# Optimization experiments

Measured on AMD Instinct MI355X. Metric: run time of the kernel, lower is better.

## Reference

```python
import jax, jax.numpy as jnp
import numpy as np

D_MODEL = 128; D_STATE = 64; HEADDIM = 32; D_CONV = 4; EXPAND = 2
D_INNER = EXPAND * D_MODEL          # 256
NHEADS = D_INNER // HEADDIM         # 8
NGROUPS = 1
D_CONV_CH = D_INNER + 2 * NGROUPS * D_STATE      # 384
D_IN_PROJ = 2 * D_INNER + 2 * NGROUPS * D_STATE + NHEADS  # 648


def _mamba2(u, Win, convw, convb, dtb, Alog, Dp, normw, Wout):
    # u: (B, L, d_model). Mamba2 forward (ngroups=1, rmsnorm gated, no in/out bias).
    B, L, _ = u.shape
    zxbcdt = u @ Win                                   # (B,L,648)
    z, xBC, dt = jnp.split(zxbcdt, [D_INNER, D_INNER + D_CONV_CH], axis=-1)
    # depthwise causal conv1d (kernel D_CONV) + SiLU
    xp = jnp.pad(xBC, ((0, 0), (D_CONV - 1, 0), (0, 0)))
    xconv = sum(xp[:, k:k + L, :] * convw[k] for k in range(D_CONV)) + convb
    xBC = jax.nn.silu(xconv)
    x, Bm, Cm = jnp.split(xBC, [D_INNER, D_INNER + NGROUPS * D_STATE], axis=-1)
    dt = jax.nn.softplus(dt + dtb)                     # (B,L,H)
    A = -jnp.exp(Alog)                                 # (H,)
    xh = x.reshape(B, L, NHEADS, HEADDIM)              # (B,L,H,P)
    dA = jnp.exp(dt * A)                               # (B,L,H)

    def step(h, inp):
        dA_t, dt_t, B_t, C_t, x_t = inp
        h = h * dA_t[:, :, None, None] + jnp.einsum('bh,bn,bhp->bhpn', dt_t, B_t, x_t)
        y = jnp.einsum('bhpn,bn->bhp', h, C_t)
        return h, y

    h0 = jnp.zeros((B, NHEADS, HEADDIM, D_STATE), dtype=u.dtype)
    xs = (jnp.moveaxis(dA, 1, 0), jnp.moveaxis(dt, 1, 0), jnp.moveaxis(Bm, 1, 0),
          jnp.moveaxis(Cm, 1, 0), jnp.moveaxis(xh, 1, 0))
    _, ys = jax.lax.scan(step, h0, xs)
    y = jnp.moveaxis(ys, 0, 1) + Dp[None, None, :, None] * xh   # skip D
    y = y.reshape(B, L, D_INNER)
    # RMSNormGated (norm_before_gate=False): rmsnorm(y * silu(z)) * weight
    y = y * jax.nn.silu(z)
    y = y * jax.lax.rsqrt(jnp.mean(y * y, axis=-1, keepdims=True) + 1e-5) * normw
    return y @ Wout


def _cross_attn(x, ctx, Wq, bq, Wk, bk, Wv, bv, Wo, bo):
    Q = x @ Wq + bq
    K = ctx @ Wk + bk
    V = ctx @ Wv + bv
    att = jax.nn.softmax(jnp.einsum('bqd,bkd->bqk', Q, K) * (D_MODEL ** -0.5), axis=-1)
    return jnp.einsum('bqk,bkd->bqd', att, V) @ Wo + bo


def setup_inputs() -> dict:
    key = jax.random.key(0)
    ks = jax.random.split(key, 8)
    B, L = 2048, 8

    def lin(k, fi, fo):
        return jax.random.normal(k, (fi, fo), jnp.float32) / np.sqrt(fi)

    def mamba_params(kseq):
        k = jax.random.split(kseq, 6)
        dt = jax.random.uniform(k[3], (NHEADS,), minval=0.001, maxval=0.1)
        return {
            'Win': lin(k[0], D_MODEL, D_IN_PROJ),
            'convw': jax.random.normal(k[1], (D_CONV, D_CONV_CH), jnp.float32) * 0.2,
            'convb': jnp.zeros((D_CONV_CH,), jnp.float32),
            'dtb': dt + jnp.log(-jnp.expm1(-dt)),  # inverse softplus
            'Alog': jnp.log(jax.random.uniform(k[4], (NHEADS,), minval=1.0, maxval=16.0)),
            'D': jnp.ones((NHEADS,), jnp.float32),
            'normw': jnp.ones((D_INNER,), jnp.float32),
            'Wout': lin(k[5], D_INNER, D_MODEL),
        }

    inp = {
        'st_feature': jax.random.normal(ks[0], (B, L, D_MODEL), jnp.float32),
        'exp_feature': jax.random.normal(ks[1], (B, L, D_MODEL), jnp.float32),
    }
    for pref, p in (('st_', mamba_params(ks[2])), ('ex_', mamba_params(ks[3]))):
        for n, v in p.items():
            inp[pref + n] = v

    def ca(kseq, pref):
        k = jax.random.split(kseq, 4)
        d = {}
        for n, kk in zip(('Wq', 'Wk', 'Wv', 'Wo'), k):
            d[pref + n] = lin(kk, D_MODEL, D_MODEL)
            d[pref + 'b' + n[1]] = jnp.zeros((D_MODEL,), jnp.float32)
        return d

    inp.update(ca(ks[4], 'cx_'))  # cross_atten_exp
    inp.update(ca(ks[5], 'cs_'))  # cross_atten_st
    inp['mlp_W'] = lin(ks[6], 8 * 2 * D_MODEL, 1024)
    inp['mlp_b'] = jnp.zeros((1024,), jnp.float32)
    return inp


def reference(st_feature, exp_feature,
              st_Win, st_convw, st_convb, st_dtb, st_Alog, st_D, st_normw, st_Wout,
              ex_Win, ex_convw, ex_convb, ex_dtb, ex_Alog, ex_D, ex_normw, ex_Wout,
              cx_Wq, cx_bq, cx_Wk, cx_bk, cx_Wv, cx_bv, cx_Wo, cx_bo,
              cs_Wq, cs_bq, cs_Wk, cs_bk, cs_Wv, cs_bv, cs_Wo, cs_bo,
              mlp_W, mlp_b):
    exp_f = _mamba2(exp_feature, ex_Win, ex_convw, ex_convb, ex_dtb, ex_Alog, ex_D, ex_normw, ex_Wout)
    st_f = _mamba2(st_feature, st_Win, st_convw, st_convb, st_dtb, st_Alog, st_D, st_normw, st_Wout)
    exp_a = _cross_attn(exp_f, st_f, cx_Wq, cx_bq, cx_Wk, cx_bk, cx_Wv, cx_bv, cx_Wo, cx_bo)
    st_a = _cross_attn(st_f, exp_f, cs_Wq, cs_bq, cs_Wk, cs_bk, cs_Wv, cs_bv, cs_Wo, cs_bo)
    x = jnp.concatenate([st_a, exp_a], axis=-1)        # (B, 8, 256)
    x = x.reshape(x.shape[0], -1)                      # (B, 2048)
    return x @ mlp_W + mlp_b
```

## Files before the change

kernel.cpp:

```cpp
#include <hip/hip_runtime.h>
#include <hip/hip_bf16.h>
#include <math.h>

#define B_SZ 2048
#define L_SEQ 8
#define DMODEL 128
#define DSTATE 64
#define HEADDIM 32
#define DCONV 4
#define DINNER 256
#define NHEADS 8
#define DCONVCH 384
#define DINPROJ 648
#define NPAD 656

typedef short bf16x8 __attribute__((ext_vector_type(8)));
typedef float floatx4 __attribute__((ext_vector_type(4)));

__device__ __forceinline__ float siluf(float x) {
    return x / (1.f + expf(-x));
}
__device__ __forceinline__ float bf2f(unsigned short h) {
    unsigned int u = ((unsigned int)h) << 16;
    return __builtin_bit_cast(float, u);
}
__device__ __forceinline__ unsigned short f2bf(float f) {
    __hip_bfloat16 b = __float2bfloat16(f);
    return __builtin_bit_cast(unsigned short, b);
}
__device__ __forceinline__ void unpack8(bf16x8 v, float* o) {
    #pragma unroll
    for (int j = 0; j < 8; ++j) o[j] = bf2f((unsigned short)v[j]);
}
__device__ __forceinline__ void gl_lds16(const unsigned short* g, unsigned short* l) {
    __builtin_amdgcn_global_load_lds(
        (const __attribute__((address_space(1))) unsigned int*)g,
        (__attribute__((address_space(3))) unsigned int*)l, 16, 0, 0);
}

__global__ __launch_bounds__(256) void prep_weights(
    const float* __restrict__ st_Win, const float* __restrict__ ex_Win,
    const float* __restrict__ st_Wout, const float* __restrict__ ex_Wout,
    const float* __restrict__ cs_Wq, const float* __restrict__ cs_Wk,
    const float* __restrict__ cs_Wv, const float* __restrict__ cs_Wo,
    const float* __restrict__ cx_Wq, const float* __restrict__ cx_Wk,
    const float* __restrict__ cx_Wv, const float* __restrict__ cx_Wo,
    const float* __restrict__ mlp_W,
    unsigned short* __restrict__ winT_st, unsigned short* __restrict__ winT_ex,
    unsigned short* __restrict__ woutT_st, unsigned short* __restrict__ woutT_ex,
    unsigned short* __restrict__ attnWT, unsigned short* __restrict__ mlpWt)
{
    __shared__ float tile[32][33];
    int blk = blockIdx.x;
    if (blk < 656) {
        const float* src = blk < 328 ? st_Win : ex_Win;
        unsigned short* dst = blk < 328 ? winT_st : winT_ex;
        int idx = (blk % 328) * 256 + threadIdx.x;
        if (idx >= NPAD * 128) return;
        int n = idx / 128, k = idx % 128;
        float v = (n < DINPROJ) ? src[k * DINPROJ + n] : 0.f;
        dst[idx] = f2bf(v);
    } else if (blk < 912) {
        const float* src = blk < 784 ? st_Wout : ex_Wout;
        unsigned short* dst = blk < 784 ? woutT_st : woutT_ex;
        int idx = ((blk - 656) % 128) * 256 + threadIdx.x;
        int n = idx / 256, k = idx % 256;
        dst[idx] = f2bf(src[k * 128 + n]);
    } else if (blk < 1424) {
        int b2 = blk - 912;
        int mat = b2 >> 6;
        const float* src = mat == 0 ? cs_Wq : mat == 1 ? cs_Wk : mat == 2 ? cs_Wv :
                           mat == 3 ? cs_Wo : mat == 4 ? cx_Wq : mat == 5 ? cx_Wk :
                           mat == 6 ? cx_Wv : cx_Wo;
        int e = (b2 & 63) * 256 + threadIdx.x;
        int n = e >> 7, k = e & 127;
        attnWT[mat * 16384 + n * 128 + k] = f2bf(src[k * 128 + n]);
    } else {
        int b2 = blk - 1424;
        int n0 = (b2 & 31) * 32, k0 = (b2 >> 5) * 32;
        const int tid = threadIdx.x;
        const int c = tid & 31, r0 = tid >> 5;
        for (int rr = r0; rr < 32; rr += 8)
            tile[rr][c] = mlp_W[(size_t)(k0 + rr) * 1024 + n0 + c];
        __syncthreads();
        for (int rr = r0; rr < 32; rr += 8)
            mlpWt[(size_t)(n0 + rr) * 2048 + k0 + c] = f2bf(tile[c][rr]);
    }
}

#define LDK 136
#define LDZ 648
#define LDY 264
__global__ __launch_bounds__(256, 4) void mamba_dual(
    const float* __restrict__ u_ex, const float* __restrict__ u_st,
    const unsigned short* __restrict__ WinT_ex, const unsigned short* __restrict__ WinT_st,
    const float* __restrict__ convw_ex, const float* __restrict__ convw_st,
    const float* __restrict__ convb_ex, const float* __restrict__ convb_st,
    const float* __restrict__ dtb_ex, const float* __restrict__ dtb_st,
    const float* __restrict__ Alog_ex, const float* __restrict__ Alog_st,
    const float* __restrict__ Dp_ex, const float* __restrict__ Dp_st,
    const float* __restrict__ normw_ex, const float* __restrict__ normw_st,
    const unsigned short* __restrict__ WoutT_ex, const unsigned short* __restrict__ WoutT_st,
    unsigned short* __restrict__ out_ex, unsigned short* __restrict__ out_st)
{
    const int which = blockIdx.x >> 10;
    const float* u = which ? u_st : u_ex;
    const unsigned short* WinT = which ? WinT_st : WinT_ex;
    const float* convw = which ? convw_st : convw_ex;
    const float* convb = which ? convb_st : convb_ex;
    const float* dtb = which ? dtb_st : dtb_ex;
    const float* Alog = which ? Alog_st : Alog_ex;
    const float* Dp = which ? Dp_st : Dp_ex;
    const float* normw = which ? normw_st : normw_ex;
    const unsigned short* WoutT = which ? WoutT_st : WoutT_ex;
    unsigned short* outf = which ? out_st : out_ex;

    const int tid = threadIdx.x;
    const int lane = tid & 63;
    const int wave = tid >> 6;
    const int l15 = lane & 15;
    const int q8 = (lane >> 4) * 8;
    const int row0 = (lane >> 4) * 4;
    const int grow0 = (blockIdx.x & 1023) * 16;

    __shared__ __align__(16) unsigned short uA[16 * LDK];
    __shared__ __align__(16) unsigned short zx[16 * LDZ];
    __shared__ __align__(16) unsigned short yb[16 * LDY];
    __shared__ float dtraw[16][8];
    __shared__ float dtv[2][8][8];
    __shared__ float cum[2][8][8];
    __shared__ float Gm[2][8][8];
    __shared__ float red[16][32];
    __shared__ float rstd[16];
    float* coefp = (float*)uA;

    for (int i = tid; i < 512; i += 256) {
        int r = i >> 5, k4 = (i & 31) * 4;
        float4 v = *(const float4*)(u + (size_t)(grow0 + r) * DMODEL + k4);
        ushort4 h;
        h.x = f2bf(v.x); h.y = f2bf(v.y); h.z = f2bf(v.z); h.w = f2bf(v.w);
        *(ushort4*)(uA + r * LDK + k4) = h;
    }
    __syncthreads();

    {
        bf16x8 af[4];
        #pragma unroll
        for (int kk = 0; kk < 4; ++kk)
            af[kk] = *(const bf16x8*)(uA + l15 * LDK + kk * 32 + q8);
        for (int nt = wave; nt < 41; nt += 4) {
            floatx4 acc = {0.f, 0.f, 0.f, 0.f};
            const unsigned short* bp = WinT + (size_t)(nt * 16 + l15) * 128 + q8;
            #pragma unroll
            for (int kk = 0; kk < 4; ++kk) {
                bf16x8 bf = *(const bf16x8*)(bp + kk * 32);
                acc = __builtin_amdgcn_mfma_f32_16x16x32_bf16(af[kk], bf, acc, 0, 0, 0);
            }
            if (nt == 40) {
                if (l15 < 8) {
                    #pragma unroll
                    for (int r = 0; r < 4; ++r)
                        dtraw[row0 + r][l15] = acc[r];
                }
            } else {
                #pragma unroll
                for (int r = 0; r < 4; ++r)
                    zx[(row0 + r) * LDZ + nt * 16 + l15] = f2bf(acc[r]);
            }
        }
    }
    __syncthreads();

    float cv[3][8];
    {
        #pragma unroll
        for (int it = 0; it < 3; ++it) {
            int i = tid + it * 256;
            int r = i / 48, g = i % 48;
            int c0 = g * 8;
            int l = r & 7, bloc = r >> 3;
            float s[8];
            float4 cb0 = *(const float4*)(convb + c0);
            float4 cb1 = *(const float4*)(convb + c0 + 4);
            s[0] = cb0.x; s[1] = cb0.y; s[2] = cb0.z; s[3] = cb0.w;
            s[4] = cb1.x; s[5] = cb1.y; s[6] = cb1.z; s[7] = cb1.w;
            #pragma unroll
            for (int k = 0; k < DCONV; ++k) {
                int lp = l + k - (DCONV - 1);
                if (lp >= 0) {
                    bf16x8 v = *(const bf16x8*)(zx + (bloc * 8 + lp) * LDZ + 256 + c0);
                    float vf[8];
                    unpack8(v, vf);
                    float4 w0 = *(const float4*)(convw + k * DCONVCH + c0);
                    float4 w1 = *(const float4*)(convw + k * DCONVCH + c0 + 4);
                    s[0] += vf[0] * w0.x; s[1] += vf[1] * w0.y;
                    s[2] += vf[2] * w0.z; s[3] += vf[3] * w0.w;
                    s[4] += vf[4] * w1.x; s[5] += vf[5] * w1.y;
                    s[6] += vf[6] * w1.z; s[7] += vf[7] * w1.w;
                }
            }
            #pragma unroll
            for (int j = 0; j < 8; ++j) cv[it][j] = siluf(s[j]);
        }
        if (tid < 128) {
            int r = tid >> 3, h = tid & 7;
            float v = dtraw[r][h] + dtb[h];
            dtv[r >> 3][r & 7][h] = (v > 20.f) ? v : log1pf(expf(v));
        }
    }
    __syncthreads();
    {
        #pragma unroll
        for (int it = 0; it < 3; ++it) {
            int i = tid + it * 256;
            int r = i / 48, c0 = (i % 48) * 8;
            bf16x8 o;
            #pragma unroll
            for (int j = 0; j < 8; ++j) o[j] = (short)f2bf(cv[it][j]);
            *(bf16x8*)(zx + r * LDZ + 256 + c0) = o;
        }
    }
    __syncthreads();

    if (tid < 128) {
        int bloc = tid >> 6, t = (tid >> 3) & 7, s = tid & 7;
        float a = 0.f;
        #pragma unroll
        for (int n = 0; n < DSTATE; n += 8) {
            bf16x8 bv = *(const bf16x8*)(zx + (bloc * 8 + s) * LDZ + 512 + n);
            bf16x8 cvv = *(const bf16x8*)(zx + (bloc * 8 + t) * LDZ + 576 + n);
            float bf_[8], cf_[8];
            unpack8(bv, bf_); unpack8(cvv, cf_);
            #pragma unroll
            for (int j = 0; j < 8; ++j) a += bf_[j] * cf_[j];
        }
        Gm[bloc][t][s] = a;
    } else if (tid < 144) {
        int j = tid - 128;
        int bloc = j >> 3, h = j & 7;
        float c = 0.f;
        for (int l = 0; l < L_SEQ; ++l) { c += dtv[bloc][l][h]; cum[bloc][l][h] = c; }
    }
    __syncthreads();

    for (int i = tid; i < 1024; i += 256) {
        int bloc = i >> 9, t = (i >> 6) & 7, s = (i >> 3) & 7, h = i & 7;
        float A = -expf(Alog[h]);
        coefp[i] = (s <= t)
            ? Gm[bloc][t][s] * expf(A * (cum[bloc][t][h] - cum[bloc][s][h])) * dtv[bloc][s][h]
            : 0.f;
    }
    __syncthreads();

    {
        #pragma unroll
        for (int it = 0; it < 2; ++it) {
            int i = tid + it * 256;
            int r = i >> 5, g = i & 31;
            int c0 = g * 8, h = g >> 2;
            int bloc = r >> 3, t = r & 7;
            float acc[8];
            {
                bf16x8 xv = *(const bf16x8*)(zx + r * LDZ + 256 + c0);
                float xf[8]; unpack8(xv, xf);
                float d = Dp[h];
                #pragma unroll
                for (int j = 0; j < 8; ++j) acc[j] = d * xf[j];
            }
            for (int s = 0; s <= t; ++s) {
                float cf = coefp[((bloc * 8 + t) * 8 + s) * 8 + h];
                bf16x8 xv = *(const bf16x8*)(zx + (bloc * 8 + s) * LDZ + 256 + c0);
                float xf[8]; unpack8(xv, xf);
                #pragma unroll
                for (int j = 0; j < 8; ++j) acc[j] += cf * xf[j];
            }
            bf16x8 zv = *(const bf16x8*)(zx + r * LDZ + c0);
            float zf[8]; unpack8(zv, zf);
            float p = 0.f;
            bf16x8 o;
            #pragma unroll
            for (int j = 0; j < 8; ++j) {
                float y = acc[j] * siluf(zf[j]);
                p += y * y;
                o[j] = (short)f2bf(y);
            }
            *(bf16x8*)(yb + r * LDY + c0) = o;
            red[r][g] = p;
        }
    }
    __syncthreads();
    if (tid < 16) {
        float s = 0.f;
        #pragma unroll
        for (int j = 0; j < 32; ++j) s += red[tid][j];
        rstd[tid] = rsqrtf(s / (float)DINNER + 1e-5f);
    }
    __syncthreads();
    {
        #pragma unroll
        for (int it = 0; it < 2; ++it) {
            int i = tid + it * 256;
            int r = i >> 5, c0 = (i & 31) * 8;
            bf16x8 v = *(const bf16x8*)(yb + r * LDY + c0);
            float vf[8]; unpack8(v, vf);
            float4 w0 = *(const float4*)(normw + c0);
            float4 w1 = *(const float4*)(normw + c0 + 4);
            float rs = rstd[r];
            bf16x8 o;
            o[0] = (short)f2bf(vf[0] * rs * w0.x); o[1] = (short)f2bf(vf[1] * rs * w0.y);
            o[2] = (short)f2bf(vf[2] * rs * w0.z); o[3] = (short)f2bf(vf[3] * rs * w0.w);
            o[4] = (short)f2bf(vf[4] * rs * w1.x); o[5] = (short)f2bf(vf[5] * rs * w1.y);
            o[6] = (short)f2bf(vf[6] * rs * w1.z); o[7] = (short)f2bf(vf[7] * rs * w1.w);
            *(bf16x8*)(yb + r * LDY + c0) = o;
        }
    }
    __syncthreads();

    {
        bf16x8 af[8];
        #pragma unroll
        for (int kk = 0; kk < 8; ++kk)
            af[kk] = *(const bf16x8*)(yb + l15 * LDY + kk * 32 + q8);
        #pragma unroll
        for (int ni = 0; ni < 2; ++ni) {
            int nt = wave * 2 + ni;
            floatx4 acc = {0.f, 0.f, 0.f, 0.f};
            const unsigned short* bp = WoutT + (size_t)(nt * 16 + l15) * 256 + q8;
            #pragma unroll
            for (int kk = 0; kk < 8; ++kk) {
                bf16x8 bf = *(const bf16x8*)(bp + kk * 32);
                acc = __builtin_amdgcn_mfma_f32_16x16x32_bf16(af[kk], bf, acc, 0, 0, 0);
            }
            #pragma unroll
            for (int r = 0; r < 4; ++r)
                outf[(size_t)(grow0 + row0 + r) * DMODEL + nt * 16 + l15] = f2bf(acc[r]);
        }
    }
}

#define ASTR 136
#define VSTR 40
#define PSTR 40
__global__ __launch_bounds__(256, 2) void attn_kernel(
    const unsigned short* __restrict__ st_f,
    const unsigned short* __restrict__ exp_f,
    const unsigned short* __restrict__ WT,
    const float* __restrict__ cs_bq, const float* __restrict__ cs_bk,
    const float* __restrict__ cs_bv, const float* __restrict__ cs_bo,
    const float* __restrict__ cx_bq, const float* __restrict__ cx_bk,
    const float* __restrict__ cx_bv, const float* __restrict__ cx_bo,
    __hip_bfloat16* __restrict__ x)
{
    const int tid = threadIdx.x;
    const int lane = tid & 63, wave = tid >> 6;
    const int l15 = lane & 15;
    const int q8 = (lane >> 4) * 8;
    const int row0 = (lane >> 4) * 4;
    const int grow0 = blockIdx.x * 32;
    const int b0 = blockIdx.x * 4;
    const float scale = 0.08838834764831845f;

    __shared__ __align__(16) unsigned short stf[32 * ASTR];
    __shared__ __align__(16) unsigned short exf[32 * ASTR];
    __shared__ __align__(16) unsigned short Qs[32 * ASTR];
    __shared__ __align__(16) unsigned short Ks[32 * ASTR];
    __shared__ __align__(16) unsigned short attv[32 * ASTR];
    __shared__ __align__(16) unsigned short Vt[128 * VSTR];
    __shared__ __align__(16) unsigned short P[32 * PSTR];
    __shared__ float Ss[32][33];

    #pragma unroll
    for (int it = 0; it < 2; ++it) {
        int i = tid + it * 256;
        int r = i >> 4, c8 = (i & 15) * 8;
        *(uint4*)(stf + r * ASTR + c8) = *(const uint4*)(st_f + (size_t)(grow0 + r) * 128 + c8);
        *(uint4*)(exf + r * ASTR + c8) = *(const uint4*)(exp_f + (size_t)(grow0 + r) * 128 + c8);
    }
    __syncthreads();

    #pragma unroll
    for (int pass = 0; pass < 2; ++pass) {
        const unsigned short* qsrc = pass ? exf : stf;
        const unsigned short* kvsrc = pass ? stf : exf;
        const unsigned short* Wq = WT + (size_t)pass * 4 * 16384;
        const unsigned short* Wk = Wq + 16384;
        const unsigned short* Wv = Wq + 32768;
        const unsigned short* Wo = Wq + 49152;
        const float* bq = pass ? cx_bq : cs_bq;
        const float* bk = pass ? cx_bk : cs_bk;
        const float* bv = pass ? cx_bv : cs_bv;
        const float* bo = pass ? cx_bo : cs_bo;

        {
            bf16x8 aq[2][4], akv[2][4];
            #pragma unroll
            for (int mt = 0; mt < 2; ++mt)
                #pragma unroll
                for (int kk = 0; kk < 4; ++kk) {
                    aq[mt][kk]  = *(const bf16x8*)(qsrc  + (mt * 16 + l15) * ASTR + kk * 32 + q8);
                    akv[mt][kk] = *(const bf16x8*)(kvsrc + (mt * 16 + l15) * ASTR + kk * 32 + q8);
                }
            #pragma unroll
            for (int ni = 0; ni < 2; ++ni) {
                int nc = (wave * 2 + ni) * 16 + l15;
                floatx4 aq0 = {0,0,0,0}, aq1 = {0,0,0,0};
                floatx4 ak0 = {0,0,0,0}, ak1 = {0,0,0,0};
                floatx4 av0 = {0,0,0,0}, av1 = {0,0,0,0};
                #pragma unroll
                for (int kk = 0; kk < 4; ++kk) {
                    bf16x8 wqf = *(const bf16x8*)(Wq + (size_t)nc * 128 + kk * 32 + q8);
                    bf16x8 wkf = *(const bf16x8*)(Wk + (size_t)nc * 128 + kk * 32 + q8);
                    bf16x8 wvf = *(const bf16x8*)(Wv + (size_t)nc * 128 + kk * 32 + q8);
                    aq0 = __builtin_amdgcn_mfma_f32_16x16x32_bf16(aq[0][kk],  wqf, aq0, 0, 0, 0);
                    aq1 = __builtin_amdgcn_mfma_f32_16x16x32_bf16(aq[1][kk],  wqf, aq1, 0, 0, 0);
                    ak0 = __builtin_amdgcn_mfma_f32_16x16x32_bf16(akv[0][kk], wkf, ak0, 0, 0, 0);
                    ak1 = __builtin_amdgcn_mfma_f32_16x16x32_bf16(akv[1][kk], wkf, ak1, 0, 0, 0);
                    av0 = __builtin_amdgcn_mfma_f32_16x16x32_bf16(akv[0][kk], wvf, av0, 0, 0, 0);
                    av1 = __builtin_amdgcn_mfma_f32_16x16x32_bf16(akv[1][kk], wvf, av1, 0, 0, 0);
                }
                float bqv = bq[nc], bkv = bk[nc], bvv = bv[nc];
                #pragma unroll
                for (int r = 0; r < 4; ++r) {
                    Qs[(row0 + r) * ASTR + nc]      = f2bf(aq0[r] + bqv);
                    Qs[(16 + row0 + r) * ASTR + nc] = f2bf(aq1[r] + bqv);
                    Ks[(row0 + r) * ASTR + nc]      = f2bf(ak0[r] + bkv);
                    Ks[(16 + row0 + r) * ASTR + nc] = f2bf(ak1[r] + bkv);
                    Vt[nc * VSTR + row0 + r]        = f2bf(av0[r] + bvv);
                    Vt[nc * VSTR + 16 + row0 + r]   = f2bf(av1[r] + bvv);
                }
            }
        }
        __syncthreads();

        {
            int mtS = wave >> 1, ntS = wave & 1;
            floatx4 s = {0,0,0,0};
            #pragma unroll
            for (int kk = 0; kk < 4; ++kk) {
                bf16x8 a = *(const bf16x8*)(Qs + (mtS * 16 + l15) * ASTR + kk * 32 + q8);
                bf16x8 b = *(const bf16x8*)(Ks + (ntS * 16 + l15) * ASTR + kk * 32 + q8);
                s = __builtin_amdgcn_mfma_f32_16x16x32_bf16(a, b, s, 0, 0, 0);
            }
            #pragma unroll
            for (int r = 0; r < 4; ++r)
                Ss[mtS * 16 + row0 + r][ntS * 16 + l15] = s[r];
        }
        __syncthreads();

        if (tid < 32) {
            int r = tid, c0 = (r >> 3) * 8;
            float v[8], mx = -1e30f;
            #pragma unroll
            for (int c = 0; c < 8; ++c) {
                v[c] = Ss[r][c0 + c] * scale;
                mx = fmaxf(mx, v[c]);
            }
            float sum = 0.f;
            #pragma unroll
            for (int c = 0; c < 8; ++c) { v[c] = expf(v[c] - mx); sum += v[c]; }
            float inv = 1.f / sum;
            #pragma unroll
            for (int c = 0; c < 32; ++c) {
                float pv = (c >= c0 && c < c0 + 8) ? v[c - c0] * inv : 0.f;
                P[r * PSTR + c] = f2bf(pv);
            }
        }
        __syncthreads();

        {
            #pragma unroll
            for (int ni = 0; ni < 2; ++ni) {
                int nc = (wave * 2 + ni) * 16 + l15;
                bf16x8 bv_ = *(const bf16x8*)(Vt + nc * VSTR + q8);
                #pragma unroll
                for (int mt = 0; mt < 2; ++mt) {
                    bf16x8 ap = *(const bf16x8*)(P + (mt * 16 + l15) * PSTR + q8);
                    floatx4 o = {0,0,0,0};
                    o = __builtin_amdgcn_mfma_f32_16x16x32_bf16(ap, bv_, o, 0, 0, 0);
                    #pragma unroll
                    for (int r = 0; r < 4; ++r)
                        attv[(mt * 16 + row0 + r) * ASTR + nc] = f2bf(o[r]);
                }
            }
        }
        __syncthreads();

        {
            bf16x8 ao[2][4];
            #pragma unroll
            for (int mt = 0; mt < 2; ++mt)
                #pragma unroll
                for (int kk = 0; kk < 4; ++kk)
                    ao[mt][kk] = *(const bf16x8*)(attv + (mt * 16 + l15) * ASTR + kk * 32 + q8);
            #pragma unroll
            for (int ni = 0; ni < 2; ++ni) {
                int nc = (wave * 2 + ni) * 16 + l15;
                floatx4 a0 = {0,0,0,0}, a1 = {0,0,0,0};
                #pragma unroll
                for (int kk = 0; kk < 4; ++kk) {
                    bf16x8 wof = *(const bf16x8*)(Wo + (size_t)nc * 128 + kk * 32 + q8);
                    a0 = __builtin_amdgcn_mfma_f32_16x16x32_bf16(ao[0][kk], wof, a0, 0, 0, 0);
                    a1 = __builtin_amdgcn_mfma_f32_16x16x32_bf16(ao[1][kk], wof, a1, 0, 0, 0);
                }
                float bov = bo[nc];
                #pragma unroll
                for (int r = 0; r < 4; ++r) {
                    int rr0 = row0 + r;
                    int rr1 = 16 + row0 + r;
                    x[(size_t)(b0 + (rr0 >> 3)) * 2048 + (rr0 & 7) * 256 + pass * 128 + nc] =
                        __float2bfloat16(a0[r] + bov);
                    x[(size_t)(b0 + (rr1 >> 3)) * 2048 + (rr1 & 7) * 256 + pass * 128 + nc] =
                        __float2bfloat16(a1[r] + bov);
                }
            }
        }
        __syncthreads();
    }
}

__global__ __launch_bounds__(256, 2) void mlp_mfma(
    const unsigned short* __restrict__ X,
    const unsigned short* __restrict__ Wt,
    const float* __restrict__ bias,
    float* __restrict__ out)
{
    __shared__ __align__(16) unsigned short As[64 * 64];
    __shared__ __align__(16) unsigned short Bs[64 * 64];
    const int tid = threadIdx.x;
    const int wave = tid >> 6, lane = tid & 63;
    const int wm = (wave >> 1) * 32, wn = (wave & 1) * 32;
    const int bm = blockIdx.y * 64, bn = blockIdx.x * 64;
    const int l15 = lane & 15, q8 = (lane >> 4) * 8;

    const int c0i = tid, c1i = tid + 256;
    const int r0s = c0i >> 3, c0s = ((c0i & 7) ^ (r0s & 7)) * 8;
    const int r1s = c1i >> 3, c1s = ((c1i & 7) ^ (r1s & 7)) * 8;
    const unsigned short* gA0 = X + (size_t)(bm + r0s) * 2048 + c0s;
    const unsigned short* gA1 = X + (size_t)(bm + r1s) * 2048 + c1s;
    const unsigned short* gB0 = Wt + (size_t)(bn + r0s) * 2048 + c0s;
    const unsigned short* gB1 = Wt + (size_t)(bn + r1s) * 2048 + c1s;
    unsigned short* lA0 = As + c0i * 8;
    unsigned short* lA1 = As + c1i * 8;
    unsigned short* lB0 = Bs + c0i * 8;
    unsigned short* lB1 = Bs + c1i * 8;

    floatx4 acc[2][2];
    #pragma unroll
    for (int i = 0; i < 2; ++i)
        #pragma unroll
        for (int j = 0; j < 2; ++j) acc[i][j] = (floatx4){0.f, 0.f, 0.f, 0.f};

    const int ra0 = wm + l15, ra1 = wm + 16 + l15;
    const int rb0 = wn + l15, rb1 = wn + 16 + l15;

    for (int k0 = 0; k0 < 2048; k0 += 64) {
        __syncthreads();
        gl_lds16(gA0 + k0, lA0);
        gl_lds16(gA1 + k0, lA1);
        gl_lds16(gB0 + k0, lB0);
        gl_lds16(gB1 + k0, lB1);
        __syncthreads();
        #pragma unroll
        for (int ks = 0; ks < 2; ++ks) {
            int xx = ks * 4 + (q8 >> 3);
            bf16x8 a0 = *(const bf16x8*)(As + (ra0 * 8 + (xx ^ (ra0 & 7))) * 8);
            bf16x8 a1 = *(const bf16x8*)(As + (ra1 * 8 + (xx ^ (ra1 & 7))) * 8);
            bf16x8 b0 = *(const bf16x8*)(Bs + (rb0 * 8 + (xx ^ (rb0 & 7))) * 8);
            bf16x8 b1 = *(const bf16x8*)(Bs + (rb1 * 8 + (xx ^ (rb1 & 7))) * 8);
            acc[0][0] = __builtin_amdgcn_mfma_f32_16x16x32_bf16(a0, b0, acc[0][0], 0, 0, 0);
            acc[0][1] = __builtin_amdgcn_mfma_f32_16x16x32_bf16(a0, b1, acc[0][1], 0, 0, 0);
            acc[1][0] = __builtin_amdgcn_mfma_f32_16x16x32_bf16(a1, b0, acc[1][0], 0, 0, 0);
            acc[1][1] = __builtin_amdgcn_mfma_f32_16x16x32_bf16(a1, b1, acc[1][1], 0, 0, 0);
        }
    }

    const int row0 = (lane >> 4) * 4;
    #pragma unroll
    for (int j = 0; j < 2; ++j) {
        int col = bn + wn + j * 16 + l15;
        float bv = bias[col];
        #pragma unroll
        for (int r = 0; r < 4; ++r) {
            out[(size_t)(bm + wm + row0 + r) * 1024 + col] = acc[0][j][r] + bv;
            out[(size_t)(bm + wm + 16 + row0 + r) * 1024 + col] = acc[1][j][r] + bv;
        }
    }
}

extern "C" void kernel_launch(void* const* d_in, const int* in_sizes, int n_in,
                              void* d_out, int out_size, void* d_ws, size_t ws_size,
                              hipStream_t stream) {
    const float* st_feature = (const float*)d_in[0];
    const float* exp_feature = (const float*)d_in[1];
    const float* st_Win = (const float*)d_in[2];
    const float* st_convw = (const float*)d_in[3];
    const float* st_convb = (const float*)d_in[4];
    const float* st_dtb = (const float*)d_in[5];
    const float* st_Alog = (const float*)d_in[6];
    const float* st_D = (const float*)d_in[7];
    const float* st_normw = (const float*)d_in[8];
    const float* st_Wout = (const float*)d_in[9];
    const float* ex_Win = (const float*)d_in[10];
    const float* ex_convw = (const float*)d_in[11];
    const float* ex_convb = (const float*)d_in[12];
    const float* ex_dtb = (const float*)d_in[13];
    const float* ex_Alog = (const float*)d_in[14];
    const float* ex_D = (const float*)d_in[15];
    const float* ex_normw = (const float*)d_in[16];
    const float* ex_Wout = (const float*)d_in[17];
    const float* cx_Wq = (const float*)d_in[18]; const float* cx_bq = (const float*)d_in[19];
    const float* cx_Wk = (const float*)d_in[20]; const float* cx_bk = (const float*)d_in[21];
    const float* cx_Wv = (const float*)d_in[22]; const float* cx_bv = (const float*)d_in[23];
    const float* cx_Wo = (const float*)d_in[24]; const float* cx_bo = (const float*)d_in[25];
    const float* cs_Wq = (const float*)d_in[26]; const float* cs_bq = (const float*)d_in[27];
    const float* cs_Wk = (const float*)d_in[28]; const float* cs_bk = (const float*)d_in[29];
    const float* cs_Wv = (const float*)d_in[30]; const float* cs_bv = (const float*)d_in[31];
    const float* cs_Wo = (const float*)d_in[32]; const float* cs_bo = (const float*)d_in[33];
    const float* mlp_W = (const float*)d_in[34];
    const float* mlp_b = (const float*)d_in[35];

    unsigned short* wsu = (unsigned short*)d_ws;
    unsigned short* st_fb  = wsu;
    unsigned short* exp_fb = st_fb + (size_t)B_SZ * L_SEQ * DMODEL;
    unsigned short* xbuf   = exp_fb + (size_t)B_SZ * L_SEQ * DMODEL;
    unsigned short* wtbuf  = xbuf + (size_t)2048 * 2048;
    unsigned short* winT_st = wtbuf + (size_t)1024 * 2048;
    unsigned short* winT_ex = winT_st + (size_t)NPAD * 128;
    unsigned short* woutT_st = winT_ex + (size_t)NPAD * 128;
    unsigned short* woutT_ex = woutT_st + (size_t)128 * 256;
    unsigned short* attnWT  = woutT_ex + (size_t)128 * 256;

    prep_weights<<<3472, 256, 0, stream>>>(
        st_Win, ex_Win, st_Wout, ex_Wout,
        cs_Wq, cs_Wk, cs_Wv, cs_Wo, cx_Wq, cx_Wk, cx_Wv, cx_Wo, mlp_W,
        winT_st, winT_ex, woutT_st, woutT_ex, attnWT, wtbuf);
    mamba_dual<<<2048, 256, 0, stream>>>(
        exp_feature, st_feature, winT_ex, winT_st,
        ex_convw, st_convw, ex_convb, st_convb,
        ex_dtb, st_dtb, ex_Alog, st_Alog, ex_D, st_D,
        ex_normw, st_normw, woutT_ex, woutT_st,
        exp_fb, st_fb);
    attn_kernel<<<B_SZ / 4, 256, 0, stream>>>(st_fb, exp_fb, attnWT,
                                              cs_bq, cs_bk, cs_bv, cs_bo,
                                              cx_bq, cx_bk, cx_bv, cx_bo,
                                              (__hip_bfloat16*)xbuf);
    {
        dim3 g(1024 / 64, 2048 / 64);
        mlp_mfma<<<g, 256, 0, stream>>>(xbuf, wtbuf, mlp_b, (float*)d_out);
    }
}
```

Baseline: 253.5 us.

## Shrink mamba LDS, parallelize cross-attn passes, double-buffer MLP GEMM loads

The mamba kernel drops its yb and red shared buffers. It keeps the gated y values in registers, reduces the RMS sums with wave shuffles instead of an LDS pass, and reuses the zx region for the normalized output. That lowers LDS use so the launch bound can rise to 5 blocks per CU. The cross-attention kernel now runs both attention directions at once, with two waves per direction, instead of two sequential passes, and it reads activations straight from global memory. The MLP GEMM double-buffers its LDS tiles so the next K-tile load is issued before the current one is computed, leaving one barrier per iteration. Risks include a possible race, since the next tile's async load into the other buffer may not be waited on before it is read, plus extra register pressure from the higher occupancy target.

```diff
diff --git a/kernel.cpp b/kernel.cpp
--- a/kernel.cpp
+++ b/kernel.cpp
@@ -91,7 +91,7 @@
 #define LDK 136
 #define LDZ 648
 #define LDY 264
-__global__ __launch_bounds__(256, 4) void mamba_dual(
+__global__ __launch_bounds__(256, 5) void mamba_dual(
     const float* __restrict__ u_ex, const float* __restrict__ u_st,
     const unsigned short* __restrict__ WinT_ex, const unsigned short* __restrict__ WinT_st,
     const float* __restrict__ convw_ex, const float* __restrict__ convw_st,
@@ -125,14 +125,13 @@
 
     __shared__ __align__(16) unsigned short uA[16 * LDK];
     __shared__ __align__(16) unsigned short zx[16 * LDZ];
-    __shared__ __align__(16) unsigned short yb[16 * LDY];
     __shared__ float dtraw[16][8];
     __shared__ float dtv[2][8][8];
     __shared__ float cum[2][8][8];
     __shared__ float Gm[2][8][8];
-    __shared__ float red[16][32];
     __shared__ float rstd[16];
     float* coefp = (float*)uA;
+    unsigned short* ybA = zx;
 
     for (int i = tid; i < 512; i += 256) {
         int r = i >> 5, k4 = (i & 31) * 4;
@@ -252,7 +251,9 @@
     }
     __syncthreads();
 
-    {
+    float yv[2][8];
+    {
+        float psum[2];
         #pragma unroll
         for (int it = 0; it < 2; ++it) {
             int i = tid + it * 256;
@@ -277,41 +278,45 @@
             bf16x8 zv = *(const bf16x8*)(zx + r * LDZ + c0);
             float zf[8]; unpack8(zv, zf);
             float p = 0.f;
-            bf16x8 o;
             #pragma unroll
             for (int j = 0; j < 8; ++j) {
                 float y = acc[j] * siluf(zf[j]);
                 p += y * y;
-                o[j] = (short)f2bf(y);
-            }
-            *(bf16x8*)(yb + r * LDY + c0) = o;
-            red[r][g] = p;
-        }
-    }
-    __syncthreads();
-    if (tid < 16) {
-        float s = 0.f;
-        #pragma unroll
-        for (int j = 0; j < 32; ++j) s += red[tid][j];
-        rstd[tid] = rsqrtf(s / (float)DINNER + 1e-5f);
-    }
-    __syncthreads();
+                yv[it][j] = y;
+            }
+            psum[it] = p;
+        }
+        #pragma unroll
+        for (int off = 16; off > 0; off >>= 1) {
+            psum[0] += __shfl_down(psum[0], off, 32);
+            psum[1] += __shfl_down(psum[1], off, 32);
+        }
+        if ((lane & 31) == 0) {
+            int r = tid >> 5;
+            rstd[r]     = rsqrtf(psum[0] * (1.f / DINNER) + 1e-5f);
+            rstd[r + 8] = rsqrtf(psum[1] * (1.f / DINNER) + 1e-5f);
+        }
+    }
+    __syncthreads();
+
     {
         #pragma unroll
         for (int it = 0; it < 2; ++it) {
             int i = tid + it * 256;
             int r = i >> 5, c0 = (i & 31) * 8;
-            bf16x8 v = *(const bf16x8*)(yb + r * LDY + c0);
-            float vf[8]; unpack8(v, vf);
+            float rs = rstd[r];
             float4 w0 = *(const float4*)(normw + c0);
             float4 w1 = *(const float4*)(normw + c0 + 4);
-            float rs = rstd[r];
             bf16x8 o;
-            o[0] = (short)f2bf(vf[0] * rs * w0.x); o[1] = (short)f2bf(vf[1] * rs * w0.y);
-            o[2] = (short)f2bf(vf[2] * rs * w0.z); o[3] = (short)f2bf(vf[3] * rs * w0.w);
-            o[4] = (short)f2bf(vf[4] * rs * w1.x); o[5] = (short)f2bf(vf[5] * rs * w1.y);
-            o[6] = (short)f2bf(vf[6] * rs * w1.z); o[7] = (short)f2bf(vf[7] * rs * w1.w);
-            *(bf16x8*)(yb + r * LDY + c0) = o;
+            o[0] = (short)f2bf(yv[it][0] * rs * w0.x);
+            o[1] = (short)f2bf(yv[it][1] * rs * w0.y);
+            o[2] = (short)f2bf(yv[it][2] * rs * w0.z);
+            o[3] = (short)f2bf(yv[it][3] * rs * w0.w);
+            o[4] = (short)f2bf(yv[it][4] * rs * w1.x);
+            o[5] = (short)f2bf(yv[it][5] * rs * w1.y);
+            o[6] = (short)f2bf(yv[it][6] * rs * w1.z);
+            o[7] = (short)f2bf(yv[it][7] * rs * w1.w);
+            *(bf16x8*)(ybA + r * LDY + c0) = o;
         }
     }
     __syncthreads();
@@ -320,7 +325,7 @@
         bf16x8 af[8];
         #pragma unroll
         for (int kk = 0; kk < 8; ++kk)
-            af[kk] = *(const bf16x8*)(yb + l15 * LDY + kk * 32 + q8);
+            af[kk] = *(const bf16x8*)(ybA + l15 * LDY + kk * 32 + q8);
         #pragma unroll
         for (int ni = 0; ni < 2; ++ni) {
             int nt = wave * 2 + ni;
@@ -353,6 +358,8 @@
 {
     const int tid = threadIdx.x;
     const int lane = tid & 63, wave = tid >> 6;
+    const int wp = wave >> 1;
+    const int wv = wave & 1;
     const int l15 = lane & 15;
     const int q8 = (lane >> 4) * 8;
     const int row0 = (lane >> 4) * 4;
@@ -360,161 +367,149 @@
     const int b0 = blockIdx.x * 4;
     const float scale = 0.08838834764831845f;
 
-    __shared__ __align__(16) unsigned short stf[32 * ASTR];
-    __shared__ __align__(16) unsigned short exf[32 * ASTR];
-    __shared__ __align__(16) unsigned short Qs[32 * ASTR];
-    __shared__ __align__(16) unsigned short Ks[32 * ASTR];
-    __shared__ __align__(16) unsigned short attv[32 * ASTR];
-    __shared__ __align__(16) unsigned short Vt[128 * VSTR];
-    __shared__ __align__(16) unsigned short P[32 * PSTR];
-    __shared__ float Ss[32][33];
-
-    #pragma unroll
-    for (int it = 0; it < 2; ++it) {
-        int i = tid + it * 256;
-        int r = i >> 4, c8 = (i & 15) * 8;
-        *(uint4*)(stf + r * ASTR + c8) = *(const uint4*)(st_f + (size_t)(grow0 + r) * 128 + c8);
-        *(uint4*)(exf + r * ASTR + c8) = *(const uint4*)(exp_f + (size_t)(grow0 + r) * 128 + c8);
-    }
-    __syncthreads();
-
-    #pragma unroll
-    for (int pass = 0; pass < 2; ++pass) {
-        const unsigned short* qsrc = pass ? exf : stf;
-        const unsigned short* kvsrc = pass ? stf : exf;
-        const unsigned short* Wq = WT + (size_t)pass * 4 * 16384;
-        const unsigned short* Wk = Wq + 16384;
-        const unsigned short* Wv = Wq + 32768;
-        const unsigned short* Wo = Wq + 49152;
-        const float* bq = pass ? cx_bq : cs_bq;
-        const float* bk = pass ? cx_bk : cs_bk;
-        const float* bv = pass ? cx_bv : cs_bv;
-        const float* bo = pass ? cx_bo : cs_bo;
-
-        {
-            bf16x8 aq[2][4], akv[2][4];
-            #pragma unroll
-            for (int mt = 0; mt < 2; ++mt)
+    __shared__ __align__(16) unsigned short QsA[2][32 * ASTR];
+    __shared__ __align__(16) unsigned short Ks[2][32 * ASTR];
+    __shared__ __align__(16) unsigned short Vt[2][128 * VSTR];
+    __shared__ __align__(16) unsigned short P[2][32 * PSTR];
+    __shared__ float Ss[2][32][33];
+
+    const unsigned short* qg = wp ? exp_f : st_f;
+    const unsigned short* kg = wp ? st_f : exp_f;
+    const unsigned short* Wq = WT + (size_t)wp * 4 * 16384;
+    const unsigned short* Wk = Wq + 16384;
+    const unsigned short* Wv = Wq + 32768;
+    const unsigned short* Wo = Wq + 49152;
+    const float* bq = wp ? cx_bq : cs_bq;
+    const float* bk = wp ? cx_bk : cs_bk;
+    const float* bv = wp ? cx_bv : cs_bv;
+    const float* bo = wp ? cx_bo : cs_bo;
+
+    {
+        bf16x8 aq[2][4], akv[2][4];
+        #pragma unroll
+        for (int mt = 0; mt < 2; ++mt)
+            #pragma unroll
+            for (int kk = 0; kk < 4; ++kk) {
+                size_t off = (size_t)(grow0 + mt * 16 + l15) * 128 + kk * 32 + q8;
+                aq[mt][kk]  = *(const bf16x8*)(qg + off);
+                akv[mt][kk] = *(const bf16x8*)(kg + off);
+            }
+        #pragma unroll
+        for (int ni = 0; ni < 4; ++ni) {
+            int nc = (wv * 4 + ni) * 16 + l15;
+            floatx4 aq0 = {0,0,0,0}, aq1 = {0,0,0,0};
+            floatx4 ak0 = {0,0,0,0}, ak1 = {0,0,0,0};
+            floatx4 av0 = {0,0,0,0}, av1 = {0,0,0,0};
+            #pragma unroll
+            for (int kk = 0; kk < 4; ++kk) {
+                bf16x8 wqf = *(const bf16x8*)(Wq + (size_t)nc * 128 + kk * 32 + q8);
+                bf16x8 wkf = *(const bf16x8*)(Wk + (size_t)nc * 128 + kk * 32 + q8);
+                bf16x8 wvf = *(const bf16x8*)(Wv + (size_t)nc * 128 + kk * 32 + q8);
+                aq0 = __builtin_amdgcn_mfma_f32_16x16x32_bf16(aq[0][kk],  wqf, aq0, 0, 0, 0);
+                aq1 = __builtin_amdgcn_mfma_f32_16x16x32_bf16(aq[1][kk],  wqf, aq1, 0, 0, 0);
+                ak0 = __builtin_amdgcn_mfma_f32_16x16x32_bf16(akv[0][kk], wkf, ak0, 0, 0, 0);
+                ak1 = __builtin_amdgcn_mfma_f32_16x16x32_bf16(akv[1][kk], wkf, ak1, 0, 0, 0);
+                av0 = __builtin_amdgcn_mfma_f32_16x16x32_bf16(akv[0][kk], wvf, av0, 0, 0, 0);
+                av1 = __builtin_amdgcn_mfma_f32_16x16x32_bf16(akv[1][kk], wvf, av1, 0, 0, 0);
+            }
+            float bqv = bq[nc], bkv = bk[nc], bvv = bv[nc];
+            #pragma unroll
+            for (int r = 0; r < 4; ++r) {
+                QsA[wp][(row0 + r) * ASTR + nc]      = f2bf(aq0[r] + bqv);
+                QsA[wp][(16 + row0 + r) * ASTR + nc] = f2bf(aq1[r] + bqv);
+                Ks[wp][(row0 + r) * ASTR + nc]       = f2bf(ak0[r] + bkv);
+                Ks[wp][(16 + row0 + r) * ASTR + nc]  = f2bf(ak1[r] + bkv);
+                Vt[wp][nc * VSTR + row0 + r]         = f2bf(av0[r] + bvv);
+                Vt[wp][nc * VSTR + 16 + row0 + r]    = f2bf(av1[r] + bvv);
+            }
+        }
+    }
+    __syncthreads();
+
+    {
+        #pragma unroll
+        for (int ntS = 0; ntS < 2; ++ntS) {
+            floatx4 s = {0,0,0,0};
+            #pragma unroll
+            for (int kk = 0; kk < 4; ++kk) {
+                bf16x8 a = *(const bf16x8*)(QsA[wp] + (wv * 16 + l15) * ASTR + kk * 32 + q8);
+                bf16x8 b = *(const bf16x8*)(Ks[wp] + (ntS * 16 + l15) * ASTR + kk * 32 + q8);
+                s = __builtin_amdgcn_mfma_f32_16x16x32_bf16(a, b, s, 0, 0, 0);
+            }
+            #pragma unroll
+            for (int r = 0; r < 4; ++r)
+                Ss[wp][wv * 16 + row0 + r][ntS * 16 + l15] = s[r];
+        }
+    }
+    __syncthreads();
+
+    if (tid < 64) {
+        int wp2 = tid >> 5, r = tid & 31, c0 = (r >> 3) * 8;
+        float v[8], mx = -1e30f;
+        #pragma unroll
+        for (int c = 0; c < 8; ++c) {
+            v[c] = Ss[wp2][r][c0 + c] * scale;
+            mx = fmaxf(mx, v[c]);
+        }
+        float sum = 0.f;
+        #pragma unroll
+        for (int c = 0; c < 8; ++c) { v[c] = expf(v[c] - mx); sum += v[c]; }
+        float inv = 1.f / sum;
+        #pragma unroll
+        for (int c = 0; c < 32; ++c) {
+            float pv = (c >= c0 && c < c0 + 8) ? v[c - c0] * inv : 0.f;
+            P[wp2][r * PSTR + c] = f2bf(pv);
+        }
+    }
+    __syncthreads();
+
+    unsigned short* attv = QsA[wp];
+    {
+        #pragma unroll
+        for (int ni = 0; ni < 4; ++ni) {
+            int nc = (wv * 4 + ni) * 16 + l15;
+            bf16x8 bv_ = *(const bf16x8*)(Vt[wp] + nc * VSTR + q8);
+            #pragma unroll
+            for (int mt = 0; mt < 2; ++mt) {
+                bf16x8 ap = *(const bf16x8*)(P[wp] + (mt * 16 + l15) * PSTR + q8);
+                floatx4 o = {0,0,0,0};
+                o = __builtin_amdgcn_mfma_f32_16x16x32_bf16(ap, bv_, o, 0, 0, 0);
                 #pragma unroll
-                for (int kk = 0; kk < 4; ++kk) {
-                    aq[mt][kk]  = *(const bf16x8*)(qsrc  + (mt * 16 + l15) * ASTR + kk * 32 + q8);
-                    akv[mt][kk] = *(const bf16x8*)(kvsrc + (mt * 16 + l15) * ASTR + kk * 32 + q8);
-                }
-            #pragma unroll
-            for (int ni = 0; ni < 2; ++ni) {
-                int nc = (wave * 2 + ni) * 16 + l15;
-                floatx4 aq0 = {0,0,0,0}, aq1 = {0,0,0,0};
-                floatx4 ak0 = {0,0,0,0}, ak1 = {0,0,0,0};
-                floatx4 av0 = {0,0,0,0}, av1 = {0,0,0,0};
-                #pragma unroll
-                for (int kk = 0; kk < 4; ++kk) {
-                    bf16x8 wqf = *(const bf16x8*)(Wq + (size_t)nc * 128 + kk * 32 + q8);
-                    bf16x8 wkf = *(const bf16x8*)(Wk + (size_t)nc * 128 + kk * 32 + q8);
-                    bf16x8 wvf = *(const bf16x8*)(Wv + (size_t)nc * 128 + kk * 32 + q8);
-                    aq0 = __builtin_amdgcn_mfma_f32_16x16x32_bf16(aq[0][kk],  wqf, aq0, 0, 0, 0);
-                    aq1 = __builtin_amdgcn_mfma_f32_16x16x32_bf16(aq[1][kk],  wqf, aq1, 0, 0, 0);
-                    ak0 = __builtin_amdgcn_mfma_f32_16x16x32_bf16(akv[0][kk], wkf, ak0, 0, 0, 0);
-                    ak1 = __builtin_amdgcn_mfma_f32_16x16x32_bf16(akv[1][kk], wkf, ak1, 0, 0, 0);
-                    av0 = __builtin_amdgcn_mfma_f32_16x16x32_bf16(akv[0][kk], wvf, av0, 0, 0, 0);
-                    av1 = __builtin_amdgcn_mfma_f32_16x16x32_bf16(akv[1][kk], wvf, av1, 0, 0, 0);
-                }
-                float bqv = bq[nc], bkv = bk[nc], bvv = bv[nc];
-                #pragma unroll
-                for (int r = 0; r < 4; ++r) {
-                    Qs[(row0 + r) * ASTR + nc]      = f2bf(aq0[r] + bqv);
-                    Qs[(16 + row0 + r) * ASTR + nc] = f2bf(aq1[r] + bqv);
-                    Ks[(row0 + r) * ASTR + nc]      = f2bf(ak0[r] + bkv);
-                    Ks[(16 + row0 + r) * ASTR + nc] = f2bf(ak1[r] + bkv);
-                    Vt[nc * VSTR + row0 + r]        = f2bf(av0[r] + bvv);
-                    Vt[nc * VSTR + 16 + row0 + r]   = f2bf(av1[r] + bvv);
-                }
-            }
-        }
-        __syncthreads();
-
-        {
-            int mtS = wave >> 1, ntS = wave & 1;
-            floatx4 s = {0,0,0,0};
+                for (int r = 0; r < 4; ++r)
+                    attv[(mt * 16 + row0 + r) * ASTR + nc] = f2bf(o[r]);
+            }
+        }
+    }
+    __syncthreads();
+
+    {
+        bf16x8 ao[2][4];
+        #pragma unroll
+        for (int mt = 0; mt < 2; ++mt)
+            #pragma unroll
+            for (int kk = 0; kk < 4; ++kk)
+                ao[mt][kk] = *(const bf16x8*)(attv + (mt * 16 + l15) * ASTR + kk * 32 + q8);
+        #pragma unroll
+        for (int ni = 0; ni < 4; ++ni) {
+            int nc = (wv * 4 + ni) * 16 + l15;
+            floatx4 a0 = {0,0,0,0}, a1 = {0,0,0,0};
             #pragma unroll
             for (int kk = 0; kk < 4; ++kk) {
-                bf16x8 a = *(const bf16x8*)(Qs + (mtS * 16 + l15) * ASTR + kk * 32 + q8);
-                bf16x8 b = *(const bf16x8*)(Ks + (ntS * 16 + l15) * ASTR + kk * 32 + q8);
-                s = __builtin_amdgcn_mfma_f32_16x16x32_bf16(a, b, s, 0, 0, 0);
-            }
-            #pragma unroll
-            for (int r = 0; r < 4; ++r)
-                Ss[mtS * 16 + row0 + r][ntS * 16 + l15] = s[r];
-        }
-        __syncthreads();
-
-        if (tid < 32) {
-            int r = tid, c0 = (r >> 3) * 8;
-            float v[8], mx = -1e30f;
-            #pragma unroll
-            for (int c = 0; c < 8; ++c) {
-                v[c] = Ss[r][c0 + c] * scale;
-                mx = fmaxf(mx, v[c]);
-            }
-            float sum = 0.f;
-            #pragma unroll
-            for (int c = 0; c < 8; ++c) { v[c] = expf(v[c] - mx); sum += v[c]; }
-            float inv = 1.f / sum;
-            #pragma unroll
-            for (int c = 0; c < 32; ++c) {
-                float pv = (c >= c0 && c < c0 + 8) ? v[c - c0] * inv : 0.f;
-                P[r * PSTR + c] = f2bf(pv);
-            }
-        }
-        __syncthreads();
-
-        {
-            #pragma unroll
-            for (int ni = 0; ni < 2; ++ni) {
-                int nc = (wave * 2 + ni) * 16 + l15;
-                bf16x8 bv_ = *(const bf16x8*)(Vt + nc * VSTR + q8);
-                #pragma unroll
-                for (int mt = 0; mt < 2; ++mt) {
-                    bf16x8 ap = *(const bf16x8*)(P + (mt * 16 + l15) * PSTR + q8);
-                    floatx4 o = {0,0,0,0};
-                    o = __builtin_amdgcn_mfma_f32_16x16x32_bf16(ap, bv_, o, 0, 0, 0);
-                    #pragma unroll
-                    for (int r = 0; r < 4; ++r)
-                        attv[(mt * 16 + row0 + r) * ASTR + nc] = f2bf(o[r]);
-                }
-            }
-        }
-        __syncthreads();
-
-        {
-            bf16x8 ao[2][4];
-            #pragma unroll
-            for (int mt = 0; mt < 2; ++mt)
-                #pragma unroll
-                for (int kk = 0; kk < 4; ++kk)
-                    ao[mt][kk] = *(const bf16x8*)(attv + (mt * 16 + l15) * ASTR + kk * 32 + q8);
-            #pragma unroll
-            for (int ni = 0; ni < 2; ++ni) {
-                int nc = (wave * 2 + ni) * 16 + l15;
-                floatx4 a0 = {0,0,0,0}, a1 = {0,0,0,0};
-                #pragma unroll
-                for (int kk = 0; kk < 4; ++kk) {
-                    bf16x8 wof = *(const bf16x8*)(Wo + (size_t)nc * 128 + kk * 32 + q8);
-                    a0 = __builtin_amdgcn_mfma_f32_16x16x32_bf16(ao[0][kk], wof, a0, 0, 0, 0);
-                    a1 = __builtin_amdgcn_mfma_f32_16x16x32_bf16(ao[1][kk], wof, a1, 0, 0, 0);
-                }
-                float bov = bo[nc];
-                #pragma unroll
-                for (int r = 0; r < 4; ++r) {
-                    int rr0 = row0 + r;
-                    int rr1 = 16 + row0 + r;
-                    x[(size_t)(b0 + (rr0 >> 3)) * 2048 + (rr0 & 7) * 256 + pass * 128 + nc] =
-                        __float2bfloat16(a0[r] + bov);
-                    x[(size_t)(b0 + (rr1 >> 3)) * 2048 + (rr1 & 7) * 256 + pass * 128 + nc] =
-                        __float2bfloat16(a1[r] + bov);
-                }
-            }
-        }
-        __syncthreads();
+                bf16x8 wof = *(const bf16x8*)(Wo + (size_t)nc * 128 + kk * 32 + q8);
+                a0 = __builtin_amdgcn_mfma_f32_16x16x32_bf16(ao[0][kk], wof, a0, 0, 0, 0);
+                a1 = __builtin_amdgcn_mfma_f32_16x16x32_bf16(ao[1][kk], wof, a1, 0, 0, 0);
+            }
+            float bov = bo[nc];
+            #pragma unroll
+            for (int r = 0; r < 4; ++r) {
+                int rr0 = row0 + r;
+                int rr1 = 16 + row0 + r;
+                x[(size_t)(b0 + (rr0 >> 3)) * 2048 + (rr0 & 7) * 256 + wp * 128 + nc] =
+                    __float2bfloat16(a0[r] + bov);
+                x[(size_t)(b0 + (rr1 >> 3)) * 2048 + (rr1 & 7) * 256 + wp * 128 + nc] =
+                    __float2bfloat16(a1[r] + bov);
+            }
+        }
     }
 }
 
@@ -524,8 +519,8 @@
     const float* __restrict__ bias,
     float* __restrict__ out)
 {
-    __shared__ __align__(16) unsigned short As[64 * 64];
-    __shared__ __align__(16) unsigned short Bs[64 * 64];
+    __shared__ __align__(16) unsigned short As[2][64 * 64];
+    __shared__ __align__(16) unsigned short Bs[2][64 * 64];
     const int tid = threadIdx.x;
     const int wave = tid >> 6, lane = tid & 63;
     const int wm = (wave >> 1) * 32, wn = (wave & 1) * 32;
@@ -539,10 +534,6 @@
     const unsigned short* gA1 = X + (size_t)(bm + r1s) * 2048 + c1s;
     const unsigned short* gB0 = Wt + (size_t)(bn + r0s) * 2048 + c0s;
     const unsigned short* gB1 = Wt + (size_t)(bn + r1s) * 2048 + c1s;
-    unsigned short* lA0 = As + c0i * 8;
-    unsigned short* lA1 = As + c1i * 8;
-    unsigned short* lB0 = Bs + c0i * 8;
-    unsigned short* lB1 = Bs + c1i * 8;
 
     floatx4 acc[2][2];
     #pragma unroll
@@ -553,25 +544,33 @@
     const int ra0 = wm + l15, ra1 = wm + 16 + l15;
     const int rb0 = wn + l15, rb1 = wn + 16 + l15;
 
+    gl_lds16(gA0, As[0] + c0i * 8);
+    gl_lds16(gA1, As[0] + c1i * 8);
+    gl_lds16(gB0, Bs[0] + c0i * 8);
+    gl_lds16(gB1, Bs[0] + c1i * 8);
+    __syncthreads();
+
     for (int k0 = 0; k0 < 2048; k0 += 64) {
-        __syncthreads();
-        gl_lds16(gA0 + k0, lA0);
-        gl_lds16(gA1 + k0, lA1);
-        gl_lds16(gB0 + k0, lB0);
-        gl_lds16(gB1 + k0, lB1);
-        __syncthreads();
+        const int cur = (k0 >> 6) & 1, nxt = cur ^ 1;
+        if (k0 + 64 < 2048) {
+            gl_lds16(gA0 + k0 + 64, As[nxt] + c0i * 8);
+            gl_lds16(gA1 + k0 + 64, As[nxt] + c1i * 8);
+            gl_lds16(gB0 + k0 + 64, Bs[nxt] + c0i * 8);
+            gl_lds16(gB1 + k0 + 64, Bs[nxt] + c1i * 8);
+        }
         #pragma unroll
         for (int ks = 0; ks < 2; ++ks) {
             int xx = ks * 4 + (q8 >> 3);
-            bf16x8 a0 = *(const bf16x8*)(As + (ra0 * 8 + (xx ^ (ra0 & 7))) * 8);
-            bf16x8 a1 = *(const bf16x8*)(As + (ra1 * 8 + (xx ^ (ra1 & 7))) * 8);
-            bf16x8 b0 = *(const bf16x8*)(Bs + (rb0 * 8 + (xx ^ (rb0 & 7))) * 8);
-            bf16x8 b1 = *(const bf16x8*)(Bs + (rb1 * 8 + (xx ^ (rb1 & 7))) * 8);
+            bf16x8 a0 = *(const bf16x8*)(As[cur] + (ra0 * 8 + (xx ^ (ra0 & 7))) * 8);
+            bf16x8 a1 = *(const bf16x8*)(As[cur] + (ra1 * 8 + (xx ^ (ra1 & 7))) * 8);
+            bf16x8 b0 = *(const bf16x8*)(Bs[cur] + (rb0 * 8 + (xx ^ (rb0 & 7))) * 8);
+            bf16x8 b1 = *(const bf16x8*)(Bs[cur] + (rb1 * 8 + (xx ^ (rb1 & 7))) * 8);
             acc[0][0] = __builtin_amdgcn_mfma_f32_16x16x32_bf16(a0, b0, acc[0][0], 0, 0, 0);
             acc[0][1] = __builtin_amdgcn_mfma_f32_16x16x32_bf16(a0, b1, acc[0][1], 0, 0, 0);
             acc[1][0] = __builtin_amdgcn_mfma_f32_16x16x32_bf16(a1, b0, acc[1][0], 0, 0, 0);
             acc[1][1] = __builtin_amdgcn_mfma_f32_16x16x32_bf16(a1, b1, acc[1][1], 0, 0, 0);
         }
+        __syncthreads();
     }
 
     const int row0 = (lane >> 4) * 4;
```

Result: slower. 263.7 us (+4.0%).
